# Performance work log

Hardware: AMD Instinct MI355X
Metric: run time of the kernel (lower is better)

Reference implementation:

```python
import jax, jax.numpy as jnp
import numpy as np

SA_LAMBDA = 1.0
IC_LAMBDA = 1.0
EPS = 1e-12  # torch F.normalize eps


def setup_inputs() -> dict:
    key = jax.random.key(0)
    k1, k2, k3, k4 = jax.random.split(key, 4)
    TF = jax.random.normal(k1, (16, 512, 32, 32), dtype=jnp.float32)
    SF = jax.random.normal(k2, (16, 512, 32, 32), dtype=jnp.float32)
    t_out = jax.random.normal(k3, (16, 21, 128, 128), dtype=jnp.float32)
    s_out = jax.random.normal(k4, (16, 21, 128, 128), dtype=jnp.float32)
    return {"TF": TF, "SF": SF, "t_out": t_out, "s_out": s_out}


def _l2_normalize_last(A):
    # matches torch.nn.functional.normalize(x, dim=2): x / max(||x||, eps)
    n = jnp.linalg.norm(A, axis=-1, keepdims=True)
    return A / jnp.maximum(n, EPS)


def _channel_weighted_spatial_gram(F4):
    # Algebraic fusion of einsum('bij,bki->bijk') + einsum('bijk,bi->bjk'):
    # ATT[b,m,n] = sum_c F[b,c,m] * F[b,c,n] * Fc[b,c]
    b, c, h, w = F4.shape
    Fc = jnp.sum(jnp.abs(F4), axis=(2, 3))          # [b, c]
    Fm = F4.reshape(b, c, h * w)                     # [b, c, M]
    A = jnp.einsum('bcm,bc,bcn->bmn', Fm, Fc, Fm)    # [b, M, M]
    return _l2_normalize_last(A)


def _normalized_channel_gram(L):
    # ICC[b,i,j] = sum_m L[b,i,m] * L[b,j,m], then L2-normalize along last dim
    G = jnp.einsum('bim,bjm->bij', L, L)
    return _l2_normalize_last(G)


def reference(TF, SF, t_out, s_out):
    b, c, h, w = TF.shape
    M = h * w
    ATT_T = _channel_weighted_spatial_gram(TF)
    ATT_S = _channel_weighted_spatial_gram(SF)
    diff = ATT_S - ATT_T
    SA_loss = SA_LAMBDA * jnp.sum(diff * diff) / (b * M ** 2)

    bb, cc, hh, ww = s_out.shape
    s_logit = s_out.reshape(bb, cc, hh * ww)
    t_logit = t_out.reshape(bb, cc, hh * ww)
    G_diff = _normalized_channel_gram(s_logit) - _normalized_channel_gram(t_logit)
    ic_loss = IC_LAMBDA * jnp.sum(G_diff * G_diff) / (cc * bb)

    return (s_out, ic_loss, SA_loss)
```

## Files before the change

kernel.cpp:

```cpp
#include <hip/hip_runtime.h>
#include <hip/hip_bf16.h>
#include <cstdint>
#include <cstddef>

typedef __bf16 bf16x8 __attribute__((ext_vector_type(8)));
typedef float f32x4 __attribute__((ext_vector_type(4)));

__device__ __forceinline__ void gload_lds16(const void* g, void* l) {
  __builtin_amdgcn_global_load_lds((const __attribute__((address_space(1))) void*)g,
                                   (__attribute__((address_space(3))) void*)l, 16, 0, 0);
}
__device__ __forceinline__ unsigned short f2bf(float x) {
  return __builtin_bit_cast(unsigned short, __float2bfloat16(x));
}
#define S_BARRIER asm volatile("s_barrier" ::: "memory")
#define WAIT_VM(N) asm volatile("s_waitcnt vmcnt(" #N ")" ::: "memory")

__global__ void fc_kernel(const float* __restrict__ TF, const float* __restrict__ SF,
                          float* __restrict__ sqrtFc) {
  int wv = threadIdx.x >> 6, lane = threadIdx.x & 63;
  int row = blockIdx.x * 4 + wv;
  const float* X = (row < 8192) ? TF : SF;
  const float* p = X + (size_t)(row & 8191) * 1024;
  float s = 0.f;
#pragma unroll
  for (int it = 0; it < 4; ++it) {
    float4 v = *reinterpret_cast<const float4*>(p + (size_t)(it * 64 + lane) * 4);
    s += fabsf(v.x) + fabsf(v.y) + fabsf(v.z) + fabsf(v.w);
  }
#pragma unroll
  for (int m = 32; m; m >>= 1) s += __shfl_xor(s, m);
  if (lane == 0) sqrtFc[row] = sqrtf(s);
}

__global__ void __launch_bounds__(256) wprep2_kernel(const float* __restrict__ TF,
                                                     const float* __restrict__ SF,
                                                     const float* __restrict__ sqrtFc,
                                                     __hip_bfloat16* __restrict__ Wt,
                                                     __hip_bfloat16* __restrict__ Ws) {
  __shared__ float lds[64][65];
  __shared__ float scale[64];
  int z = blockIdx.z;
  int t = z >> 4, b = z & 15;
  int m0 = blockIdx.x * 64, c0 = blockIdx.y * 64;
  const float* Xg = (t ? SF : TF) + (size_t)b * 524288;
  __hip_bfloat16* Wg = (t ? Ws : Wt) + (size_t)b * 524288;
  int tid = threadIdx.x;
  if (tid < 64) scale[tid] = sqrtFc[t * 8192 + b * 512 + c0 + tid];
#pragma unroll
  for (int i = 0; i < 4; ++i) {
    int v = i * 256 + tid;
    int r = v >> 4, q = v & 15;
    *reinterpret_cast<float4*>(&lds[r][q * 4]) =
        *reinterpret_cast<const float4*>(Xg + (size_t)(c0 + r) * 1024 + m0 + q * 4);
  }
  __syncthreads();
#pragma unroll
  for (int jj = 0; jj < 2; ++jj) {
    int m = jj * 32 + (tid >> 3), oct = tid & 7;
    union { unsigned short h[8]; uint4 u; } pk;
#pragma unroll
    for (int k = 0; k < 8; ++k) {
      int c = oct * 8 + k;
      pk.h[k] = f2bf(lds[c][m] * scale[c]);
    }
    *reinterpret_cast<uint4*>(Wg + (size_t)(m0 + m) * 512 + c0 + oct * 8) = pk.u;
  }
}

__global__ void __launch_bounds__(256, 2) syrk_fused_kernel(
    const __hip_bfloat16* __restrict__ Wt, const __hip_bfloat16* __restrict__ Ws,
    float* __restrict__ nT, float* __restrict__ nS, float* __restrict__ cross) {
  __shared__ __hip_bfloat16 AL[2][128 * 64];
  __shared__ __hip_bfloat16 BL[2][128 * 64];
  int bid = blockIdx.x;
  int j = (bid & 7) * 72 + (bid >> 3);
  int b = j / 36, pair = j % 36;
  int bx = pair, tm = 0;
  while (bx >= 8 - tm) { bx -= 8 - tm; ++tm; }
  int tn = tm + bx;
  bool diag = (tm == tn);
  const __hip_bfloat16* WTb = Wt + (size_t)b * 524288;
  const __hip_bfloat16* WSb = Ws + (size_t)b * 524288;
  const __hip_bfloat16* ATp = WTb + (size_t)tm * 65536;
  const __hip_bfloat16* ASp = WSb + (size_t)tm * 65536;
  const __hip_bfloat16* BTp = WTb + (size_t)tn * 65536;
  const __hip_bfloat16* BSp = WSb + (size_t)tn * 65536;

  const int tid = threadIdx.x;
  const int lane = tid & 63, wv = tid >> 6;
  const int wr = wv >> 1, wc = wv & 1;
  const int g = lane >> 4, c0 = lane & 15, cx = c0 & 7;

  int offs[4], dst[4];
#pragma unroll
  for (int i = 0; i < 4; ++i) {
    int ci = i * 256 + tid;
    int row = ci >> 3, slot = ci & 7;
    offs[i] = row * 512 + (slot ^ (row & 7)) * 8;
    dst[i] = (i * 256 + wv * 64) * 8;
  }

  f32x4 accT[4][4], accS[4][4];
#pragma unroll
  for (int mi = 0; mi < 4; ++mi)
#pragma unroll
    for (int ni = 0; ni < 4; ++ni) {
      accT[mi][ni] = (f32x4){0.f, 0.f, 0.f, 0.f};
      accS[mi][ni] = (f32x4){0.f, 0.f, 0.f, 0.f};
    }

  auto stage = [&](int s, int buf) {
    int kt = (s & 7) * 64;
    const __hip_bfloat16* Ab = (s < 8) ? ATp : ASp;
    const __hip_bfloat16* Bb = (s < 8) ? BTp : BSp;
#pragma unroll
    for (int i = 0; i < 4; ++i) {
      gload_lds16(Ab + offs[i] + kt, &AL[buf][dst[i]]);
      if (!diag) gload_lds16(Bb + offs[i] + kt, &BL[buf][dst[i]]);
    }
  };

  stage(0, 0);
#pragma unroll
  for (int s = 0; s < 16; ++s) {
    int buf = s & 1;
    if (s < 15) {
      stage(s + 1, buf ^ 1);
      if (diag) { WAIT_VM(4); } else { WAIT_VM(8); }
    } else {
      WAIT_VM(0);
    }
    S_BARRIER;
    const __hip_bfloat16* Ab = AL[buf];
    const __hip_bfloat16* Bb = diag ? AL[buf] : BL[buf];
#pragma unroll
    for (int kk = 0; kk < 2; ++kk) {
      int ck = ((kk * 4 + g) ^ cx) * 8;
      bf16x8 av[4], bv[4];
#pragma unroll
      for (int mi = 0; mi < 4; ++mi)
        av[mi] = *reinterpret_cast<const bf16x8*>(Ab + (wr * 64 + mi * 16 + c0) * 64 + ck);
#pragma unroll
      for (int ni = 0; ni < 4; ++ni)
        bv[ni] = *reinterpret_cast<const bf16x8*>(Bb + (wc * 64 + ni * 16 + c0) * 64 + ck);
      __builtin_amdgcn_s_setprio(1);
      if (s < 8) {
#pragma unroll
        for (int mi = 0; mi < 4; ++mi)
#pragma unroll
          for (int ni = 0; ni < 4; ++ni)
            accT[mi][ni] = __builtin_amdgcn_mfma_f32_16x16x32_bf16(av[mi], bv[ni], accT[mi][ni], 0, 0, 0);
      } else {
#pragma unroll
        for (int mi = 0; mi < 4; ++mi)
#pragma unroll
          for (int ni = 0; ni < 4; ++ni)
            accS[mi][ni] = __builtin_amdgcn_mfma_f32_16x16x32_bf16(av[mi], bv[ni], accS[mi][ni], 0, 0, 0);
      }
      __builtin_amdgcn_s_setprio(0);
    }
    if (s < 15) S_BARRIER;
  }

  float* pT = nT + (size_t)b * 1024;
  float* pS = nS + (size_t)b * 1024;
  float* pC = cross + (size_t)b * 1024;
#pragma unroll
  for (int mi = 0; mi < 4; ++mi)
#pragma unroll
    for (int r = 0; r < 4; ++r) {
      float sT = 0.f, sS = 0.f, sC = 0.f;
#pragma unroll
      for (int ni = 0; ni < 4; ++ni) {
        float tv = accT[mi][ni][r], sv = accS[mi][ni][r];
        sT += tv * tv; sS += sv * sv; sC += tv * sv;
      }
#pragma unroll
      for (int msk = 1; msk < 16; msk <<= 1) {
        sT += __shfl_xor(sT, msk); sS += __shfl_xor(sS, msk); sC += __shfl_xor(sC, msk);
      }
      if (c0 == 0) {
        int m = tm * 128 + wr * 64 + mi * 16 + g * 4 + r;
        atomicAdd(pT + m, sT); atomicAdd(pS + m, sS); atomicAdd(pC + m, sC);
      }
    }
  if (!diag) {
#pragma unroll
    for (int ni = 0; ni < 4; ++ni) {
      float sT = 0.f, sS = 0.f, sC = 0.f;
#pragma unroll
      for (int mi = 0; mi < 4; ++mi)
#pragma unroll
        for (int r = 0; r < 4; ++r) {
          float tv = accT[mi][ni][r], sv = accS[mi][ni][r];
          sT += tv * tv; sS += sv * sv; sC += tv * sv;
        }
      sT += __shfl_xor(sT, 16); sS += __shfl_xor(sS, 16); sC += __shfl_xor(sC, 16);
      sT += __shfl_xor(sT, 32); sS += __shfl_xor(sS, 32); sC += __shfl_xor(sC, 32);
      if (g == 0) {
        int n = tn * 128 + wc * 64 + ni * 16 + c0;
        atomicAdd(pT + n, sT); atomicAdd(pS + n, sS); atomicAdd(pC + n, sC);
      }
    }
  }
}

__global__ void __launch_bounds__(512) icgram4_kernel(const float* __restrict__ t_out,
                                                      const float* __restrict__ s_out,
                                                      float* __restrict__ G) {
  __shared__ float lds[21 * 260];
  __shared__ float Gs[441];
  int chunk = blockIdx.x;
  int z = blockIdx.y;
  int t = z >> 4, bb = z & 15;
  const float* L = (t ? s_out : t_out) + (size_t)bb * 344064 + (size_t)chunk * 256;
  int tid = threadIdx.x;
  for (int i = tid; i < 441; i += 512) Gs[i] = 0.f;
  for (int idx = tid; idx < 21 * 64; idx += 512) {
    int r = idx >> 6, c = idx & 63;
    *reinterpret_cast<float4*>(&lds[r * 260 + c * 4]) =
        *reinterpret_cast<const float4*>(L + (size_t)r * 16384 + c * 4);
  }
  __syncthreads();
  int wv = tid >> 6, lane = tid & 63;
  for (int sp = wv; sp < 66; sp += 8) {
    int pp = sp, gi = 0;
    while (pp >= 11 - gi) { pp -= 11 - gi; ++gi; }
    int gj = gi + pp;
    int i0 = 2 * gi, j0 = 2 * gj;
    bool i1v = (i0 + 1 < 21), j1v = (j0 + 1 < 21);
    const float4* Ri0 = reinterpret_cast<const float4*>(&lds[i0 * 260]);
    const float4* Ri1 = reinterpret_cast<const float4*>(&lds[(i1v ? i0 + 1 : i0) * 260]);
    const float4* Rj0 = reinterpret_cast<const float4*>(&lds[j0 * 260]);
    const float4* Rj1 = reinterpret_cast<const float4*>(&lds[(j1v ? j0 + 1 : j0) * 260]);
    float4 a0 = Ri0[lane], a1 = Ri1[lane];
    float4 b0 = Rj0[lane], b1 = Rj1[lane];
    float s00 = a0.x * b0.x + a0.y * b0.y + a0.z * b0.z + a0.w * b0.w;
    float s01 = a0.x * b1.x + a0.y * b1.y + a0.z * b1.z + a0.w * b1.w;
    float s10 = a1.x * b0.x + a1.y * b0.y + a1.z * b0.z + a1.w * b0.w;
    float s11 = a1.x * b1.x + a1.y * b1.y + a1.z * b1.z + a1.w * b1.w;
    s00 += __shfl_xor(s00, 1); s00 += __shfl_xor(s00, 2);
    s01 += __shfl_xor(s01, 1); s01 += __shfl_xor(s01, 2);
    s10 += __shfl_xor(s10, 1); s10 += __shfl_xor(s10, 2);
    s11 += __shfl_xor(s11, 1); s11 += __shfl_xor(s11, 2);
    int q = lane & 3;
    float sq = (q == 0) ? s00 : (q == 1) ? s01 : (q == 2) ? s10 : s11;
    sq += __shfl_xor(sq, 4); sq += __shfl_xor(sq, 8);
    sq += __shfl_xor(sq, 16); sq += __shfl_xor(sq, 32);
    if (lane < 4) {
      bool ok = (lane == 0) || (lane == 1 && j1v) ||
                (lane == 2 && i1v && gi != gj) || (lane == 3 && i1v && j1v);
      int ii = (lane >> 1) ? i0 + 1 : i0;
      int jj = (lane & 1) ? j0 + 1 : j0;
      if (ok) atomicAdd(&Gs[ii * 21 + jj], sq);
    }
  }
  __syncthreads();
  float* Gz = G + (size_t)z * 441;
  for (int i = tid; i < 441; i += 512) {
    float v = Gs[i];
    if (v != 0.f) atomicAdd(&Gz[i], v);
  }
}

__global__ void finalize_kernel(const float* __restrict__ G, const float* __restrict__ nT,
                                const float* __restrict__ nS, const float* __restrict__ cross,
                                float* __restrict__ out2) {
  __shared__ float red[16];
  int tid = threadIdx.x;
  float sa = 0.f;
#pragma unroll
  for (int it = 0; it < 4; ++it) {
    int i4 = it * 1024 + tid;
    float4 a = reinterpret_cast<const float4*>(nT)[i4];
    float4 s4 = reinterpret_cast<const float4*>(nS)[i4];
    float4 c4 = reinterpret_cast<const float4*>(cross)[i4];
#pragma unroll
    for (int k = 0; k < 4; ++k) {
      float a1 = (&a.x)[k], s1 = (&s4.x)[k], c1 = (&c4.x)[k];
      float NT = fmaxf(sqrtf(a1), 1e-12f), NS = fmaxf(sqrtf(s1), 1e-12f);
      sa += a1 / (NT * NT) + s1 / (NS * NS) - 2.f * c1 / (NT * NS);
    }
  }
  float ic = 0.f;
  if (tid < 336) {
    int b = tid / 21, i = tid % 21;
    const float* gt = G + (size_t)b * 441;
    const float* gs = G + (size_t)(16 + b) * 441;
    float nt = 0.f, ns = 0.f;
    for (int j = 0; j < 21; ++j) {
      int idx2 = (i <= j) ? i * 21 + j : j * 21 + i;
      float vt = gt[idx2], vs = gs[idx2];
      nt += vt * vt; ns += vs * vs;
    }
    float rt = 1.f / fmaxf(sqrtf(nt), 1e-12f);
    float rs = 1.f / fmaxf(sqrtf(ns), 1e-12f);
    for (int j = 0; j < 21; ++j) {
      int idx2 = (i <= j) ? i * 21 + j : j * 21 + i;
      float d = gs[idx2] * rs - gt[idx2] * rt;
      ic += d * d;
    }
  }
  int lane = tid & 63, wv = tid >> 6;
#pragma unroll
  for (int m = 32; m; m >>= 1) { sa += __shfl_xor(sa, m); ic += __shfl_xor(ic, m); }
  if (lane == 0) red[wv] = sa;
  __syncthreads();
  if (tid == 0) { float s = 0.f; for (int w = 0; w < 16; ++w) s += red[w]; out2[1] = s * (1.0f / 16777216.0f); }
  __syncthreads();
  if (lane == 0) red[wv] = ic;
  __syncthreads();
  if (tid == 0) { float s = 0.f; for (int w = 0; w < 16; ++w) s += red[w]; out2[0] = s * (1.0f / 336.0f); }
}

extern "C" void kernel_launch(void* const* d_in, const int* in_sizes, int n_in,
                              void* d_out, int out_size, void* d_ws, size_t ws_size,
                              hipStream_t stream) {
  const float* TF = (const float*)d_in[0];
  const float* SF = (const float*)d_in[1];
  const float* t_out = (const float*)d_in[2];
  const float* s_out = (const float*)d_in[3];
  float* out = (float*)d_out;
  char* ws = (char*)d_ws;

  float* nT = (float*)(ws + 0);
  float* nS = (float*)(ws + 65536);
  float* cross = (float*)(ws + 131072);
  float* G = (float*)(ws + 196608);
  float* sqrtFc = (float*)(ws + 253184);
  __hip_bfloat16* Wt = (__hip_bfloat16*)(ws + 318720);
  __hip_bfloat16* Ws = (__hip_bfloat16*)(ws + 318720 + 16777216);

  (void)hipMemsetAsync(ws, 0, 253056, stream);
  (void)hipMemcpyAsync(d_out, (const void*)s_out, (size_t)5505024 * 4,
                       hipMemcpyDeviceToDevice, stream);

  fc_kernel<<<4096, 256, 0, stream>>>(TF, SF, sqrtFc);
  wprep2_kernel<<<dim3(16, 8, 32), 256, 0, stream>>>(TF, SF, sqrtFc, Wt, Ws);
  syrk_fused_kernel<<<576, 256, 0, stream>>>(Wt, Ws, nT, nS, cross);
  icgram4_kernel<<<dim3(64, 32), 512, 0, stream>>>(t_out, s_out, G);
  finalize_kernel<<<1, 1024, 0, stream>>>(G, nT, nS, cross, out + 5505024);
}
```

Baseline: 127.6 us.

## Merge SYRK and IC-gram kernels into one launch and fold s_out copy in

The SYRK tile GEMM and the IC channel-gram kernel now run as two block ranges of a single launch sharing a 64KB shared buffer. The gram blocks use 256 threads instead of 512. The device-to-device copy of s_out into the output is dropped; the gram blocks that already read s_out write it back out as they load it. This removes a launch and a separate 22MB memcpy pass and lets the memory-bound gram work overlap the MFMA-bound SYRK blocks. The cost is the larger shared-memory footprint for the gram blocks and fewer waves per gram block.

```diff
diff --git a/kernel.cpp b/kernel.cpp
--- a/kernel.cpp
+++ b/kernel.cpp
@@ -68,199 +68,203 @@
   }
 }
 
-__global__ void __launch_bounds__(256, 2) syrk_fused_kernel(
+__global__ void __launch_bounds__(256, 2) fused_kernel(
     const __hip_bfloat16* __restrict__ Wt, const __hip_bfloat16* __restrict__ Ws,
-    float* __restrict__ nT, float* __restrict__ nS, float* __restrict__ cross) {
-  __shared__ __hip_bfloat16 AL[2][128 * 64];
-  __shared__ __hip_bfloat16 BL[2][128 * 64];
-  int bid = blockIdx.x;
-  int j = (bid & 7) * 72 + (bid >> 3);
-  int b = j / 36, pair = j % 36;
-  int bx = pair, tm = 0;
-  while (bx >= 8 - tm) { bx -= 8 - tm; ++tm; }
-  int tn = tm + bx;
-  bool diag = (tm == tn);
-  const __hip_bfloat16* WTb = Wt + (size_t)b * 524288;
-  const __hip_bfloat16* WSb = Ws + (size_t)b * 524288;
-  const __hip_bfloat16* ATp = WTb + (size_t)tm * 65536;
-  const __hip_bfloat16* ASp = WSb + (size_t)tm * 65536;
-  const __hip_bfloat16* BTp = WTb + (size_t)tn * 65536;
-  const __hip_bfloat16* BSp = WSb + (size_t)tn * 65536;
-
+    float* __restrict__ nT, float* __restrict__ nS, float* __restrict__ cross,
+    const float* __restrict__ t_out, const float* __restrict__ s_out,
+    float* __restrict__ G, float* __restrict__ outcpy) {
+  __shared__ __align__(16) char smem[65536];
   const int tid = threadIdx.x;
-  const int lane = tid & 63, wv = tid >> 6;
-  const int wr = wv >> 1, wc = wv & 1;
-  const int g = lane >> 4, c0 = lane & 15, cx = c0 & 7;
-
-  int offs[4], dst[4];
-#pragma unroll
-  for (int i = 0; i < 4; ++i) {
-    int ci = i * 256 + tid;
-    int row = ci >> 3, slot = ci & 7;
-    offs[i] = row * 512 + (slot ^ (row & 7)) * 8;
-    dst[i] = (i * 256 + wv * 64) * 8;
-  }
-
-  f32x4 accT[4][4], accS[4][4];
-#pragma unroll
-  for (int mi = 0; mi < 4; ++mi)
-#pragma unroll
-    for (int ni = 0; ni < 4; ++ni) {
-      accT[mi][ni] = (f32x4){0.f, 0.f, 0.f, 0.f};
-      accS[mi][ni] = (f32x4){0.f, 0.f, 0.f, 0.f};
-    }
-
-  auto stage = [&](int s, int buf) {
-    int kt = (s & 7) * 64;
-    const __hip_bfloat16* Ab = (s < 8) ? ATp : ASp;
-    const __hip_bfloat16* Bb = (s < 8) ? BTp : BSp;
+
+  if (blockIdx.x < 576) {
+    __hip_bfloat16* AL = reinterpret_cast<__hip_bfloat16*>(smem);
+    __hip_bfloat16* BL = reinterpret_cast<__hip_bfloat16*>(smem) + 16384;
+    int bid = blockIdx.x;
+    int j = (bid & 7) * 72 + (bid >> 3);
+    int b = j / 36, pair = j % 36;
+    int bx = pair, tm = 0;
+    while (bx >= 8 - tm) { bx -= 8 - tm; ++tm; }
+    int tn = tm + bx;
+    bool diag = (tm == tn);
+    const __hip_bfloat16* WTb = Wt + (size_t)b * 524288;
+    const __hip_bfloat16* WSb = Ws + (size_t)b * 524288;
+    const __hip_bfloat16* ATp = WTb + (size_t)tm * 65536;
+    const __hip_bfloat16* ASp = WSb + (size_t)tm * 65536;
+    const __hip_bfloat16* BTp = WTb + (size_t)tn * 65536;
+    const __hip_bfloat16* BSp = WSb + (size_t)tn * 65536;
+
+    const int lane = tid & 63, wv = tid >> 6;
+    const int wr = wv >> 1, wc = wv & 1;
+    const int g = lane >> 4, c0 = lane & 15, cx = c0 & 7;
+
+    int offs[4], dst[4];
 #pragma unroll
     for (int i = 0; i < 4; ++i) {
-      gload_lds16(Ab + offs[i] + kt, &AL[buf][dst[i]]);
-      if (!diag) gload_lds16(Bb + offs[i] + kt, &BL[buf][dst[i]]);
-    }
-  };
-
-  stage(0, 0);
-#pragma unroll
-  for (int s = 0; s < 16; ++s) {
-    int buf = s & 1;
-    if (s < 15) {
-      stage(s + 1, buf ^ 1);
-      if (diag) { WAIT_VM(4); } else { WAIT_VM(8); }
-    } else {
-      WAIT_VM(0);
-    }
-    S_BARRIER;
-    const __hip_bfloat16* Ab = AL[buf];
-    const __hip_bfloat16* Bb = diag ? AL[buf] : BL[buf];
-#pragma unroll
-    for (int kk = 0; kk < 2; ++kk) {
-      int ck = ((kk * 4 + g) ^ cx) * 8;
-      bf16x8 av[4], bv[4];
-#pragma unroll
-      for (int mi = 0; mi < 4; ++mi)
-        av[mi] = *reinterpret_cast<const bf16x8*>(Ab + (wr * 64 + mi * 16 + c0) * 64 + ck);
-#pragma unroll
-      for (int ni = 0; ni < 4; ++ni)
-        bv[ni] = *reinterpret_cast<const bf16x8*>(Bb + (wc * 64 + ni * 16 + c0) * 64 + ck);
-      __builtin_amdgcn_s_setprio(1);
-      if (s < 8) {
+      int ci = i * 256 + tid;
+      int row = ci >> 3, slot = ci & 7;
+      offs[i] = row * 512 + (slot ^ (row & 7)) * 8;
+      dst[i] = (i * 256 + wv * 64) * 8;
+    }
+
+    f32x4 accT[4][4], accS[4][4];
+#pragma unroll
+    for (int mi = 0; mi < 4; ++mi)
+#pragma unroll
+      for (int ni = 0; ni < 4; ++ni) {
+        accT[mi][ni] = (f32x4){0.f, 0.f, 0.f, 0.f};
+        accS[mi][ni] = (f32x4){0.f, 0.f, 0.f, 0.f};
+      }
+
+    auto stage = [&](int s, int buf) {
+      int kt = (s & 7) * 64;
+      const __hip_bfloat16* Ab = (s < 8) ? ATp : ASp;
+      const __hip_bfloat16* Bb = (s < 8) ? BTp : BSp;
+#pragma unroll
+      for (int i = 0; i < 4; ++i) {
+        gload_lds16(Ab + offs[i] + kt, AL + buf * 8192 + dst[i]);
+        if (!diag) gload_lds16(Bb + offs[i] + kt, BL + buf * 8192 + dst[i]);
+      }
+    };
+
+    stage(0, 0);
+#pragma unroll
+    for (int s = 0; s < 16; ++s) {
+      int buf = s & 1;
+      if (s < 15) {
+        stage(s + 1, buf ^ 1);
+        if (diag) { WAIT_VM(4); } else { WAIT_VM(8); }
+      } else {
+        WAIT_VM(0);
+      }
+      S_BARRIER;
+      const __hip_bfloat16* Ab = AL + buf * 8192;
+      const __hip_bfloat16* Bb = diag ? Ab : (BL + buf * 8192);
+#pragma unroll
+      for (int kk = 0; kk < 2; ++kk) {
+        int ck = ((kk * 4 + g) ^ cx) * 8;
+        bf16x8 av[4], bv[4];
 #pragma unroll
         for (int mi = 0; mi < 4; ++mi)
-#pragma unroll
-          for (int ni = 0; ni < 4; ++ni)
-            accT[mi][ni] = __builtin_amdgcn_mfma_f32_16x16x32_bf16(av[mi], bv[ni], accT[mi][ni], 0, 0, 0);
-      } else {
-#pragma unroll
-        for (int mi = 0; mi < 4; ++mi)
-#pragma unroll
-          for (int ni = 0; ni < 4; ++ni)
-            accS[mi][ni] = __builtin_amdgcn_mfma_f32_16x16x32_bf16(av[mi], bv[ni], accS[mi][ni], 0, 0, 0);
-      }
-      __builtin_amdgcn_s_setprio(0);
-    }
-    if (s < 15) S_BARRIER;
-  }
-
-  float* pT = nT + (size_t)b * 1024;
-  float* pS = nS + (size_t)b * 1024;
-  float* pC = cross + (size_t)b * 1024;
-#pragma unroll
-  for (int mi = 0; mi < 4; ++mi)
-#pragma unroll
-    for (int r = 0; r < 4; ++r) {
-      float sT = 0.f, sS = 0.f, sC = 0.f;
-#pragma unroll
-      for (int ni = 0; ni < 4; ++ni) {
-        float tv = accT[mi][ni][r], sv = accS[mi][ni][r];
-        sT += tv * tv; sS += sv * sv; sC += tv * sv;
-      }
-#pragma unroll
-      for (int msk = 1; msk < 16; msk <<= 1) {
-        sT += __shfl_xor(sT, msk); sS += __shfl_xor(sS, msk); sC += __shfl_xor(sC, msk);
-      }
-      if (c0 == 0) {
-        int m = tm * 128 + wr * 64 + mi * 16 + g * 4 + r;
-        atomicAdd(pT + m, sT); atomicAdd(pS + m, sS); atomicAdd(pC + m, sC);
-      }
-    }
-  if (!diag) {
-#pragma unroll
-    for (int ni = 0; ni < 4; ++ni) {
-      float sT = 0.f, sS = 0.f, sC = 0.f;
-#pragma unroll
-      for (int mi = 0; mi < 4; ++mi)
-#pragma unroll
-        for (int r = 0; r < 4; ++r) {
+          av[mi] = *reinterpret_cast<const bf16x8*>(Ab + (wr * 64 + mi * 16 + c0) * 64 + ck);
+#pragma unroll
+        for (int ni = 0; ni < 4; ++ni)
+          bv[ni] = *reinterpret_cast<const bf16x8*>(Bb + (wc * 64 + ni * 16 + c0) * 64 + ck);
+        __builtin_amdgcn_s_setprio(1);
+        if (s < 8) {
+#pragma unroll
+          for (int mi = 0; mi < 4; ++mi)
+#pragma unroll
+            for (int ni = 0; ni < 4; ++ni)
+              accT[mi][ni] = __builtin_amdgcn_mfma_f32_16x16x32_bf16(av[mi], bv[ni], accT[mi][ni], 0, 0, 0);
+        } else {
+#pragma unroll
+          for (int mi = 0; mi < 4; ++mi)
+#pragma unroll
+            for (int ni = 0; ni < 4; ++ni)
+              accS[mi][ni] = __builtin_amdgcn_mfma_f32_16x16x32_bf16(av[mi], bv[ni], accS[mi][ni], 0, 0, 0);
+        }
+        __builtin_amdgcn_s_setprio(0);
+      }
+      if (s < 15) S_BARRIER;
+    }
+
+    float* pT = nT + (size_t)b * 1024;
+    float* pS = nS + (size_t)b * 1024;
+    float* pC = cross + (size_t)b * 1024;
+#pragma unroll
+    for (int mi = 0; mi < 4; ++mi)
+#pragma unroll
+      for (int r = 0; r < 4; ++r) {
+        float sT = 0.f, sS = 0.f, sC = 0.f;
+#pragma unroll
+        for (int ni = 0; ni < 4; ++ni) {
           float tv = accT[mi][ni][r], sv = accS[mi][ni][r];
           sT += tv * tv; sS += sv * sv; sC += tv * sv;
         }
-      sT += __shfl_xor(sT, 16); sS += __shfl_xor(sS, 16); sC += __shfl_xor(sC, 16);
-      sT += __shfl_xor(sT, 32); sS += __shfl_xor(sS, 32); sC += __shfl_xor(sC, 32);
-      if (g == 0) {
-        int n = tn * 128 + wc * 64 + ni * 16 + c0;
-        atomicAdd(pT + n, sT); atomicAdd(pS + n, sS); atomicAdd(pC + n, sC);
-      }
-    }
-  }
-}
-
-__global__ void __launch_bounds__(512) icgram4_kernel(const float* __restrict__ t_out,
-                                                      const float* __restrict__ s_out,
-                                                      float* __restrict__ G) {
-  __shared__ float lds[21 * 260];
-  __shared__ float Gs[441];
-  int chunk = blockIdx.x;
-  int z = blockIdx.y;
-  int t = z >> 4, bb = z & 15;
-  const float* L = (t ? s_out : t_out) + (size_t)bb * 344064 + (size_t)chunk * 256;
-  int tid = threadIdx.x;
-  for (int i = tid; i < 441; i += 512) Gs[i] = 0.f;
-  for (int idx = tid; idx < 21 * 64; idx += 512) {
-    int r = idx >> 6, c = idx & 63;
-    *reinterpret_cast<float4*>(&lds[r * 260 + c * 4]) =
-        *reinterpret_cast<const float4*>(L + (size_t)r * 16384 + c * 4);
-  }
-  __syncthreads();
-  int wv = tid >> 6, lane = tid & 63;
-  for (int sp = wv; sp < 66; sp += 8) {
-    int pp = sp, gi = 0;
-    while (pp >= 11 - gi) { pp -= 11 - gi; ++gi; }
-    int gj = gi + pp;
-    int i0 = 2 * gi, j0 = 2 * gj;
-    bool i1v = (i0 + 1 < 21), j1v = (j0 + 1 < 21);
-    const float4* Ri0 = reinterpret_cast<const float4*>(&lds[i0 * 260]);
-    const float4* Ri1 = reinterpret_cast<const float4*>(&lds[(i1v ? i0 + 1 : i0) * 260]);
-    const float4* Rj0 = reinterpret_cast<const float4*>(&lds[j0 * 260]);
-    const float4* Rj1 = reinterpret_cast<const float4*>(&lds[(j1v ? j0 + 1 : j0) * 260]);
-    float4 a0 = Ri0[lane], a1 = Ri1[lane];
-    float4 b0 = Rj0[lane], b1 = Rj1[lane];
-    float s00 = a0.x * b0.x + a0.y * b0.y + a0.z * b0.z + a0.w * b0.w;
-    float s01 = a0.x * b1.x + a0.y * b1.y + a0.z * b1.z + a0.w * b1.w;
-    float s10 = a1.x * b0.x + a1.y * b0.y + a1.z * b0.z + a1.w * b0.w;
-    float s11 = a1.x * b1.x + a1.y * b1.y + a1.z * b1.z + a1.w * b1.w;
-    s00 += __shfl_xor(s00, 1); s00 += __shfl_xor(s00, 2);
-    s01 += __shfl_xor(s01, 1); s01 += __shfl_xor(s01, 2);
-    s10 += __shfl_xor(s10, 1); s10 += __shfl_xor(s10, 2);
-    s11 += __shfl_xor(s11, 1); s11 += __shfl_xor(s11, 2);
-    int q = lane & 3;
-    float sq = (q == 0) ? s00 : (q == 1) ? s01 : (q == 2) ? s10 : s11;
-    sq += __shfl_xor(sq, 4); sq += __shfl_xor(sq, 8);
-    sq += __shfl_xor(sq, 16); sq += __shfl_xor(sq, 32);
-    if (lane < 4) {
-      bool ok = (lane == 0) || (lane == 1 && j1v) ||
-                (lane == 2 && i1v && gi != gj) || (lane == 3 && i1v && j1v);
-      int ii = (lane >> 1) ? i0 + 1 : i0;
-      int jj = (lane & 1) ? j0 + 1 : j0;
-      if (ok) atomicAdd(&Gs[ii * 21 + jj], sq);
-    }
-  }
-  __syncthreads();
-  float* Gz = G + (size_t)z * 441;
-  for (int i = tid; i < 441; i += 512) {
-    float v = Gs[i];
-    if (v != 0.f) atomicAdd(&Gz[i], v);
+#pragma unroll
+        for (int msk = 1; msk < 16; msk <<= 1) {
+          sT += __shfl_xor(sT, msk); sS += __shfl_xor(sS, msk); sC += __shfl_xor(sC, msk);
+        }
+        if (c0 == 0) {
+          int m = tm * 128 + wr * 64 + mi * 16 + g * 4 + r;
+          atomicAdd(pT + m, sT); atomicAdd(pS + m, sS); atomicAdd(pC + m, sC);
+        }
+      }
+    if (!diag) {
+#pragma unroll
+      for (int ni = 0; ni < 4; ++ni) {
+        float sT = 0.f, sS = 0.f, sC = 0.f;
+#pragma unroll
+        for (int mi = 0; mi < 4; ++mi)
+#pragma unroll
+          for (int r = 0; r < 4; ++r) {
+            float tv = accT[mi][ni][r], sv = accS[mi][ni][r];
+            sT += tv * tv; sS += sv * sv; sC += tv * sv;
+          }
+        sT += __shfl_xor(sT, 16); sS += __shfl_xor(sS, 16); sC += __shfl_xor(sC, 16);
+        sT += __shfl_xor(sT, 32); sS += __shfl_xor(sS, 32); sC += __shfl_xor(sC, 32);
+        if (g == 0) {
+          int n = tn * 128 + wc * 64 + ni * 16 + c0;
+          atomicAdd(pT + n, sT); atomicAdd(pS + n, sS); atomicAdd(pC + n, sC);
+        }
+      }
+    }
+  } else {
+    float* lds = reinterpret_cast<float*>(smem);
+    float* Gs = reinterpret_cast<float*>(smem + 21840);
+    int bi = blockIdx.x - 576;
+    int chunk = bi & 63;
+    int z = bi >> 6;
+    int t = z >> 4, bb = z & 15;
+    const float* L = (t ? s_out : t_out) + (size_t)bb * 344064 + (size_t)chunk * 256;
+    float* O = outcpy + (size_t)bb * 344064 + (size_t)chunk * 256;
+    for (int i = tid; i < 441; i += 256) Gs[i] = 0.f;
+    for (int idx = tid; idx < 21 * 64; idx += 256) {
+      int r = idx >> 6, c = idx & 63;
+      float4 v = *reinterpret_cast<const float4*>(L + (size_t)r * 16384 + c * 4);
+      if (t) *reinterpret_cast<float4*>(O + (size_t)r * 16384 + c * 4) = v;
+      *reinterpret_cast<float4*>(&lds[r * 260 + c * 4]) = v;
+    }
+    __syncthreads();
+    int wv = tid >> 6, lane = tid & 63;
+    for (int sp = wv; sp < 66; sp += 4) {
+      int pp = sp, gi = 0;
+      while (pp >= 11 - gi) { pp -= 11 - gi; ++gi; }
+      int gj = gi + pp;
+      int i0 = 2 * gi, j0 = 2 * gj;
+      bool i1v = (i0 + 1 < 21), j1v = (j0 + 1 < 21);
+      const float4* Ri0 = reinterpret_cast<const float4*>(&lds[i0 * 260]);
+      const float4* Ri1 = reinterpret_cast<const float4*>(&lds[(i1v ? i0 + 1 : i0) * 260]);
+      const float4* Rj0 = reinterpret_cast<const float4*>(&lds[j0 * 260]);
+      const float4* Rj1 = reinterpret_cast<const float4*>(&lds[(j1v ? j0 + 1 : j0) * 260]);
+      float4 a0 = Ri0[lane], a1 = Ri1[lane];
+      float4 b0 = Rj0[lane], b1 = Rj1[lane];
+      float s00 = a0.x * b0.x + a0.y * b0.y + a0.z * b0.z + a0.w * b0.w;
+      float s01 = a0.x * b1.x + a0.y * b1.y + a0.z * b1.z + a0.w * b1.w;
+      float s10 = a1.x * b0.x + a1.y * b0.y + a1.z * b0.z + a1.w * b0.w;
+      float s11 = a1.x * b1.x + a1.y * b1.y + a1.z * b1.z + a1.w * b1.w;
+      s00 += __shfl_xor(s00, 1); s00 += __shfl_xor(s00, 2);
+      s01 += __shfl_xor(s01, 1); s01 += __shfl_xor(s01, 2);
+      s10 += __shfl_xor(s10, 1); s10 += __shfl_xor(s10, 2);
+      s11 += __shfl_xor(s11, 1); s11 += __shfl_xor(s11, 2);
+      int q = lane & 3;
+      float sq = (q == 0) ? s00 : (q == 1) ? s01 : (q == 2) ? s10 : s11;
+      sq += __shfl_xor(sq, 4); sq += __shfl_xor(sq, 8);
+      sq += __shfl_xor(sq, 16); sq += __shfl_xor(sq, 32);
+      if (lane < 4) {
+        bool ok = (lane == 0) || (lane == 1 && j1v) ||
+                  (lane == 2 && i1v && gi != gj) || (lane == 3 && i1v && j1v);
+        int ii = (lane >> 1) ? i0 + 1 : i0;
+        int jj = (lane & 1) ? j0 + 1 : j0;
+        if (ok) atomicAdd(&Gs[ii * 21 + jj], sq);
+      }
+    }
+    __syncthreads();
+    float* Gz = G + (size_t)z * 441;
+    for (int i = tid; i < 441; i += 256) {
+      float v = Gs[i];
+      if (v != 0.f) atomicAdd(&Gz[i], v);
+    }
   }
 }
 
@@ -333,12 +337,9 @@
   __hip_bfloat16* Ws = (__hip_bfloat16*)(ws + 318720 + 16777216);
 
   (void)hipMemsetAsync(ws, 0, 253056, stream);
-  (void)hipMemcpyAsync(d_out, (const void*)s_out, (size_t)5505024 * 4,
-                       hipMemcpyDeviceToDevice, stream);
 
   fc_kernel<<<4096, 256, 0, stream>>>(TF, SF, sqrtFc);
   wprep2_kernel<<<dim3(16, 8, 32), 256, 0, stream>>>(TF, SF, sqrtFc, Wt, Ws);
-  syrk_fused_kernel<<<576, 256, 0, stream>>>(Wt, Ws, nT, nS, cross);
-  icgram4_kernel<<<dim3(64, 32), 512, 0, stream>>>(t_out, s_out, G);
+  fused_kernel<<<2624, 256, 0, stream>>>(Wt, Ws, nT, nS, cross, t_out, s_out, G, out);
   finalize_kernel<<<1, 1024, 0, stream>>>(G, nT, nS, cross, out + 5505024);
 }
```

Result: slower. 133.6 us (+4.7%).
